# Performance work log

Measured on AMD Instinct MI355X. Metric: run time of the kernel, lower is better.

## Reference

```python
import jax, jax.numpy as jnp
import numpy as np

MAX_LORAS = 8
IN_SIZE = 4096
OUT_SIZE = 4096
B, S = 8, 1024


def setup_inputs() -> dict:
    key = jax.random.key(0)
    k1, k2, k3 = jax.random.split(key, 3)
    x = jax.random.normal(k1, (B, S, IN_SIZE), dtype=jnp.float32)
    adapter_ids = jax.random.randint(k2, (B,), 0, MAX_LORAS, dtype=jnp.int64)
    # memory_transpose=True layout: [max_loras, input_size, output_size]
    weight = jax.random.normal(k3, (MAX_LORAS, IN_SIZE, OUT_SIZE), dtype=jnp.float32) * 0.02
    return {"x": x, "adapter_ids": adapter_ids, "weight": weight}


def reference(x, adapter_ids, weight):
    # per-batch-row adapter weight gather: [B, in, out]
    w = weight[adapter_ids]
    # einsum 'bij,bjk->bik' (memory_transpose=True path)
    out = jnp.einsum('bsi,bio->bso', x, w)
    # reduce_from_tensor_model_parallel_region is identity on a single device
    return out
```

## Files before the change

kernel.cpp:

```cpp
#include <hip/hip_runtime.h>
#include <hip/hip_bf16.h>

typedef __attribute__((ext_vector_type(8))) short short8;
typedef __attribute__((ext_vector_type(4))) float f32x4;

constexpr int S_DIM   = 1024;
constexpr int IN_DIM  = 4096;
constexpr int OUT_DIM = 4096;
constexpr int NLORA   = 8;

typedef __attribute__((address_space(3))) unsigned char lds_byte_t;
typedef const __attribute__((address_space(1))) unsigned char glb_byte_t;

__device__ __forceinline__ unsigned short f2bf(float a) {
    union { __hip_bfloat16 h; unsigned short u; } c;
    c.h = __float2bfloat16(a);
    return c.u;
}
__device__ __forceinline__ unsigned int bf2pk(float a, float b) {
    return (unsigned int)f2bf(a) | ((unsigned int)f2bf(b) << 16);
}

constexpr int WBLKS = NLORA * 64 * 64;
constexpr int XBLKS = 2048;

__global__ __launch_bounds__(256)
void prep_all(const float* __restrict__ w, unsigned short* __restrict__ wt,
              const float* __restrict__ x, unsigned short* __restrict__ xb,
              const int* __restrict__ aids, int nb, int n8) {
    const int bid = blockIdx.x;
    const int tid = threadIdx.x;

    if (bid >= WBLKS) {
        const int xb0 = bid - WBLKS;
        const int stride = XBLKS * 256;
        for (int i = xb0 * 256 + tid; i < n8; i += stride) {
            const size_t o = (size_t)i * 8;
            f32x4 v0 = *reinterpret_cast<const f32x4*>(x + o);
            f32x4 v1 = *reinterpret_cast<const f32x4*>(x + o + 4);
            uint4 d;
            d.x = bf2pk(v0[0], v0[1]);
            d.y = bf2pk(v0[2], v0[3]);
            d.z = bf2pk(v1[0], v1[1]);
            d.w = bf2pk(v1[2], v1[3]);
            *reinterpret_cast<uint4*>(xb + o) = d;
        }
        return;
    }

    const int a = bid >> 12;
    bool used = false;
    for (int i = 0; i < nb; ++i) used |= (aids[i] == a);
    if (!used) return;

    const int r  = bid & 4095;
    const int n0 = (r & 63) * 64;
    const int k0 = (r >> 6) * 64;

    __shared__ __align__(16) unsigned short t[64][72];
    const float* wb = w + (size_t)a * IN_DIM * OUT_DIM;

    const int nl = (tid & 15) * 4;
    #pragma unroll
    for (int p = 0; p < 4; ++p) {
        const int kl = p * 16 + (tid >> 4);
        f32x4 v = *reinterpret_cast<const f32x4*>(wb + (size_t)(k0 + kl) * OUT_DIM + n0 + nl);
        t[nl + 0][kl] = f2bf(v[0]);
        t[nl + 1][kl] = f2bf(v[1]);
        t[nl + 2][kl] = f2bf(v[2]);
        t[nl + 3][kl] = f2bf(v[3]);
    }
    __syncthreads();
    unsigned short* wtb = wt + (size_t)a * IN_DIM * OUT_DIM;
    const int chunk = tid & 7;
    #pragma unroll
    for (int q = 0; q < 2; ++q) {
        const int row = q * 32 + (tid >> 3);
        uint4 d = *reinterpret_cast<const uint4*>(&t[row][chunk * 8]);
        *reinterpret_cast<uint4*>(wtb + (size_t)(n0 + row) * IN_DIM + k0 + chunk * 8) = d;
    }
}

constexpr int BM = 256;
constexpr int BN = 256;
constexpr int BK = 64;
constexpr int NT = IN_DIM / BK;

__global__ __launch_bounds__(512, 2)
void gemm8p(const unsigned short* __restrict__ xb, const unsigned short* __restrict__ wt,
            const int* __restrict__ aids, float* __restrict__ out) {
    __shared__ __align__(16) unsigned char lds[2][65536];

    const int bid = blockIdx.x;
    const int swz = (bid & 7) * 64 + (bid >> 3);
    const int bz  = swz >> 6;
    const int rem = swz & 63;
    const int by  = rem >> 4;
    const int bx  = rem & 15;

    const int tid  = threadIdx.x;
    const int lane = tid & 63;
    const int wid  = tid >> 6;
    const int bm0  = by * BM;
    const int bn0  = bx * BN;
    const int aid  = aids[bz];

    const unsigned short* Ab = xb + ((size_t)bz * S_DIM + bm0) * IN_DIM;
    const unsigned short* Bb = wt + (size_t)aid * IN_DIM * OUT_DIM + (size_t)bn0 * IN_DIM;

    const int wr  = (wid >> 2) * 128;
    const int wc  = (wid & 3) * 64;
    const int l15 = lane & 15;
    const int lk  = lane >> 4;

    const int rl   = lane >> 3;
    const int ksrc = ((lane & 7) ^ rl) << 3;

    f32x4 acc[8][4] = {};

    auto stageA = [&](int buf, int k0, int g) {
        #pragma unroll
        for (int c = 0; c < 2; ++c) {
            const int chunk = c * 16 + g * 8 + wid;
            const int row   = chunk * 8 + rl;
            __builtin_amdgcn_global_load_lds(
                (glb_byte_t*)(Ab + (size_t)row * IN_DIM + k0 + ksrc),
                (lds_byte_t*)(&lds[buf][chunk * 1024]), 16, 0, 0);
        }
    };
    auto stageB = [&](int buf, int k0, int g) {
        #pragma unroll
        for (int c = 0; c < 2; ++c) {
            const int chunk = (wid >> 1) * 8 + g * 4 + (wid & 1) * 2 + c;
            const int row   = chunk * 8 + rl;
            __builtin_amdgcn_global_load_lds(
                (glb_byte_t*)(Bb + (size_t)row * IN_DIM + k0 + ksrc),
                (lds_byte_t*)(&lds[buf][32768 + chunk * 1024]), 16, 0, 0);
        }
    };

    auto readA = [&](int buf, int mh, short8 (&af)[4][2]) {
        #pragma unroll
        for (int i = 0; i < 4; ++i) {
            const int row = wr + mh * 64 + i * 16 + l15;
            #pragma unroll
            for (int kc = 0; kc < 2; ++kc) {
                const int kb = kc * 64 + lk * 16;
                af[i][kc] = *reinterpret_cast<const short8*>(
                    &lds[buf][row * 128 + (kb ^ ((row & 7) << 4))]);
            }
        }
    };
    auto readB = [&](int buf, int np, short8 (&bf)[2][2]) {
        #pragma unroll
        for (int nn = 0; nn < 2; ++nn) {
            const int row = wc + np * 32 + nn * 16 + l15;
            #pragma unroll
            for (int kc = 0; kc < 2; ++kc) {
                const int kb = kc * 64 + lk * 16;
                bf[nn][kc] = *reinterpret_cast<const short8*>(
                    &lds[buf][32768 + row * 128 + (kb ^ ((row & 7) << 4))]);
            }
        }
    };

    auto qmfma = [&](short8 (&af)[4][2], short8 (&bf)[2][2], int mh, int np) {
        __builtin_amdgcn_s_setprio(1);
        #pragma unroll
        for (int i = 0; i < 4; ++i)
            #pragma unroll
            for (int nn = 0; nn < 2; ++nn)
                #pragma unroll
                for (int kc = 0; kc < 2; ++kc)
                    acc[mh * 4 + i][np * 2 + nn] = __builtin_amdgcn_mfma_f32_16x16x32_bf16(
                        af[i][kc], bf[nn][kc], acc[mh * 4 + i][np * 2 + nn], 0, 0, 0);
        __builtin_amdgcn_s_setprio(0);
    };

    stageA(0, 0, 0); stageA(0, 0, 1); stageB(0, 0, 0); stageB(0, 0, 1);
    stageA(1, BK, 0); stageA(1, BK, 1); stageB(1, BK, 0); stageB(1, BK, 1);
    asm volatile("s_waitcnt vmcnt(8)" ::: "memory");
    __builtin_amdgcn_sched_barrier(0);
    __builtin_amdgcn_s_barrier();

    short8 a0[4][2], a1[4][2], b0[2][2], b1[2][2];

    #pragma unroll 1
    for (int j = 0; j < NT; ++j) {
        const int rb = j & 1;
        const int k2 = (j + 2) * BK;
        const bool pre = (j < NT - 2);

        readA(rb, 0, a0);
        readB(rb, 0, b0);
        __builtin_amdgcn_s_barrier();
        qmfma(a0, b0, 0, 0);
        __builtin_amdgcn_s_barrier();

        readB(rb, 1, b1);
        if (pre) stageB(rb, k2, 0);
        __builtin_amdgcn_sched_barrier(0);
        __builtin_amdgcn_s_barrier();
        qmfma(a0, b1, 0, 1);
        __builtin_amdgcn_s_barrier();

        readA(rb, 1, a1);
        if (pre) stageA(rb, k2, 0);
        __builtin_amdgcn_sched_barrier(0);
        __builtin_amdgcn_s_barrier();
        qmfma(a1, b1, 1, 1);
        __builtin_amdgcn_s_barrier();

        if (pre) {
            stageB(rb, k2, 1);
            stageA(rb, k2, 1);
            asm volatile("s_waitcnt vmcnt(8)" ::: "memory");
        } else if (j == NT - 2) {
            asm volatile("s_waitcnt vmcnt(0)" ::: "memory");
        }
        __builtin_amdgcn_sched_barrier(0);
        __builtin_amdgcn_s_barrier();
        qmfma(a1, b0, 1, 0);
        __builtin_amdgcn_s_barrier();
    }

    float* obase = out + ((size_t)bz * S_DIM + bm0 + wr) * OUT_DIM + bn0 + wc;
    #pragma unroll
    for (int m = 0; m < 8; ++m) {
        #pragma unroll
        for (int n = 0; n < 4; ++n) {
            const int col = n * 16 + l15;
            #pragma unroll
            for (int r = 0; r < 4; ++r) {
                obase[(size_t)(m * 16 + lk * 4 + r) * OUT_DIM + col] = acc[m][n][r];
            }
        }
    }
}

constexpr int TMf = 128, TNf = 128, TKf = 64;
__global__ __launch_bounds__(256, 2)
void mlora_gemm(const float* __restrict__ x, const int* __restrict__ aids,
                const float* __restrict__ w, float* __restrict__ out) {
    __shared__ __align__(16) unsigned char Asf[TMf * TKf * 2];
    __shared__ __align__(16) unsigned char Bsf[TNf * TKf * 2];

    const int tid  = threadIdx.x;
    const int lane = tid & 63;
    const int wid  = tid >> 6;
    const int bn0  = blockIdx.x * TNf;
    const int bm0  = blockIdx.y * TMf;
    const int bb   = blockIdx.z;
    const int aid  = aids[bb];

    const float* Abase = x + ((size_t)bb * S_DIM + bm0) * IN_DIM;
    const float* Bbase = w + (size_t)aid * IN_DIM * OUT_DIM + bn0;

    const int wr = (wid >> 1) * 64;
    const int wc = (wid & 1) * 64;

    f32x4 acc[4][4] = {};

    const int a_row4 = tid >> 4;
    const int a_k    = (tid & 15) * 4;
    const int b_n  = tid & 127;
    const int b_k0 = (tid >> 7) * 8;
    const int l15 = lane & 15;
    const int lk  = lane >> 4;

    for (int k0 = 0; k0 < IN_DIM; k0 += TKf) {
        #pragma unroll
        for (int p = 0; p < 8; ++p) {
            const int row = p * 16 + a_row4;
            f32x4 v = *reinterpret_cast<const f32x4*>(Abase + (size_t)row * IN_DIM + (k0 + a_k));
            uint2 d;
            d.x = bf2pk(v[0], v[1]);
            d.y = bf2pk(v[2], v[3]);
            const int off = row * (TKf * 2) + ((a_k * 2) ^ ((row & 7) << 4));
            *reinterpret_cast<uint2*>(&Asf[off]) = d;
        }
        {
            const float* bp = Bbase + (size_t)(k0 + b_k0) * OUT_DIM + b_n;
            #pragma unroll
            for (int g = 0; g < 4; ++g) {
                float f0 = bp[(size_t)(g * 16 + 0) * OUT_DIM];
                float f1 = bp[(size_t)(g * 16 + 1) * OUT_DIM];
                float f2 = bp[(size_t)(g * 16 + 2) * OUT_DIM];
                float f3 = bp[(size_t)(g * 16 + 3) * OUT_DIM];
                float f4 = bp[(size_t)(g * 16 + 4) * OUT_DIM];
                float f5 = bp[(size_t)(g * 16 + 5) * OUT_DIM];
                float f6 = bp[(size_t)(g * 16 + 6) * OUT_DIM];
                float f7 = bp[(size_t)(g * 16 + 7) * OUT_DIM];
                uint4 d;
                d.x = bf2pk(f0, f1);
                d.y = bf2pk(f2, f3);
                d.z = bf2pk(f4, f5);
                d.w = bf2pk(f6, f7);
                const int ks = b_k0 + g * 16;
                const int off = b_n * (TKf * 2) + ((ks * 2) ^ ((b_n & 7) << 4));
                *reinterpret_cast<uint4*>(&Bsf[off]) = d;
            }
        }
        __syncthreads();
        #pragma unroll
        for (int kc = 0; kc < 2; ++kc) {
            const int kbyte = kc * 64 + lk * 16;
            short8 af[4], bfr[4];
            #pragma unroll
            for (int m = 0; m < 4; ++m) {
                const int row = wr + m * 16 + l15;
                af[m] = *reinterpret_cast<const short8*>(&Asf[row * (TKf * 2) + (kbyte ^ ((row & 7) << 4))]);
            }
            #pragma unroll
            for (int n = 0; n < 4; ++n) {
                const int row = wc + n * 16 + l15;
                bfr[n] = *reinterpret_cast<const short8*>(&Bsf[row * (TKf * 2) + (kbyte ^ ((row & 7) << 4))]);
            }
            #pragma unroll
            for (int m = 0; m < 4; ++m) {
                #pragma unroll
                for (int n = 0; n < 4; ++n) {
                    acc[m][n] = __builtin_amdgcn_mfma_f32_16x16x32_bf16(af[m], bfr[n], acc[m][n], 0, 0, 0);
                }
            }
        }
        __syncthreads();
    }

    float* obase = out + ((size_t)bb * S_DIM + bm0 + wr) * OUT_DIM + bn0 + wc;
    #pragma unroll
    for (int m = 0; m < 4; ++m) {
        #pragma unroll
        for (int n = 0; n < 4; ++n) {
            const int col = n * 16 + l15;
            #pragma unroll
            for (int r = 0; r < 4; ++r) {
                obase[(size_t)(m * 16 + lk * 4 + r) * OUT_DIM + col] = acc[m][n][r];
            }
        }
    }
}

extern "C" void kernel_launch(void* const* d_in, const int* in_sizes, int n_in,
                              void* d_out, int out_size, void* d_ws, size_t ws_size,
                              hipStream_t stream) {
    const float* x    = (const float*)d_in[0];
    const int*   aids = (const int*)d_in[1];
    const float* w    = (const float*)d_in[2];
    float* out = (float*)d_out;
    const int nb = in_sizes[1];

    const size_t WT_BYTES = (size_t)NLORA * IN_DIM * OUT_DIM * 2;
    const size_t XB_BYTES = (size_t)nb * S_DIM * IN_DIM * 2;

    if (ws_size >= WT_BYTES + XB_BYTES) {
        unsigned short* wt = (unsigned short*)d_ws;
        unsigned short* xbuf = (unsigned short*)((char*)d_ws + WT_BYTES);

        const int n8 = nb * S_DIM * IN_DIM / 8;
        prep_all<<<WBLKS + XBLKS, 256, 0, stream>>>(w, wt, x, xbuf, aids, nb, n8);

        const int nwg = nb * (S_DIM / BM) * (OUT_DIM / BN);
        gemm8p<<<nwg, 512, 0, stream>>>(xbuf, wt, aids, out);
    } else {
        dim3 grid(OUT_DIM / TNf, S_DIM / TMf, nb);
        mlora_gemm<<<grid, 256, 0, stream>>>(x, aids, w, out);
    }
}
```

Before: 356.3 us.

## Fuse x fp32-to-bf16 conversion into GEMM A-tile staging

```diff
diff --git a/kernel.cpp b/kernel.cpp
--- a/kernel.cpp
+++ b/kernel.cpp
@@ -22,31 +22,12 @@
 }
 
 constexpr int WBLKS = NLORA * 64 * 64;
-constexpr int XBLKS = 2048;
 
 __global__ __launch_bounds__(256)
-void prep_all(const float* __restrict__ w, unsigned short* __restrict__ wt,
-              const float* __restrict__ x, unsigned short* __restrict__ xb,
-              const int* __restrict__ aids, int nb, int n8) {
+void prep_w(const float* __restrict__ w, unsigned short* __restrict__ wt,
+            const int* __restrict__ aids, int nb) {
     const int bid = blockIdx.x;
     const int tid = threadIdx.x;
-
-    if (bid >= WBLKS) {
-        const int xb0 = bid - WBLKS;
-        const int stride = XBLKS * 256;
-        for (int i = xb0 * 256 + tid; i < n8; i += stride) {
-            const size_t o = (size_t)i * 8;
-            f32x4 v0 = *reinterpret_cast<const f32x4*>(x + o);
-            f32x4 v1 = *reinterpret_cast<const f32x4*>(x + o + 4);
-            uint4 d;
-            d.x = bf2pk(v0[0], v0[1]);
-            d.y = bf2pk(v0[2], v0[3]);
-            d.z = bf2pk(v1[0], v1[1]);
-            d.w = bf2pk(v1[2], v1[3]);
-            *reinterpret_cast<uint4*>(xb + o) = d;
-        }
-        return;
-    }
 
     const int a = bid >> 12;
     bool used = false;
@@ -87,7 +68,7 @@
 constexpr int NT = IN_DIM / BK;
 
 __global__ __launch_bounds__(512, 2)
-void gemm8p(const unsigned short* __restrict__ xb, const unsigned short* __restrict__ wt,
+void gemm8p(const float* __restrict__ x, const unsigned short* __restrict__ wt,
             const int* __restrict__ aids, float* __restrict__ out) {
     __shared__ __align__(16) unsigned char lds[2][65536];
 
@@ -105,37 +86,51 @@
     const int bn0  = bx * BN;
     const int aid  = aids[bz];
 
-    const unsigned short* Ab = xb + ((size_t)bz * S_DIM + bm0) * IN_DIM;
+    const float* Ax = x + ((size_t)bz * S_DIM + bm0) * IN_DIM;
     const unsigned short* Bb = wt + (size_t)aid * IN_DIM * OUT_DIM + (size_t)bn0 * IN_DIM;
 
     const int wr  = (wid >> 2) * 128;
     const int wc  = (wid & 3) * 64;
     const int l15 = lane & 15;
     const int lk  = lane >> 4;
-
-    const int rl   = lane >> 3;
-    const int ksrc = ((lane & 7) ^ rl) << 3;
+    const int rl  = lane >> 3;
+    const int l7  = lane & 7;
+    const int ksrcB = (l7 ^ rl) << 3;
 
     f32x4 acc[8][4] = {};
 
-    auto stageA = [&](int buf, int k0, int g) {
-        #pragma unroll
-        for (int c = 0; c < 2; ++c) {
-            const int chunk = c * 16 + g * 8 + wid;
-            const int row   = chunk * 8 + rl;
-            __builtin_amdgcn_global_load_lds(
-                (glb_byte_t*)(Ab + (size_t)row * IN_DIM + k0 + ksrc),
-                (lds_byte_t*)(&lds[buf][chunk * 1024]), 16, 0, 0);
-        }
-    };
     auto stageB = [&](int buf, int k0, int g) {
         #pragma unroll
         for (int c = 0; c < 2; ++c) {
             const int chunk = (wid >> 1) * 8 + g * 4 + (wid & 1) * 2 + c;
             const int row   = chunk * 8 + rl;
             __builtin_amdgcn_global_load_lds(
-                (glb_byte_t*)(Bb + (size_t)row * IN_DIM + k0 + ksrc),
+                (glb_byte_t*)(Bb + (size_t)row * IN_DIM + k0 + ksrcB),
                 (lds_byte_t*)(&lds[buf][32768 + chunk * 1024]), 16, 0, 0);
+        }
+    };
+
+    auto issueXA = [&](int k0, int g, f32x4 (&v)[4]) {
+        #pragma unroll
+        for (int c = 0; c < 2; ++c) {
+            const int chunk = c * 16 + g * 8 + wid;
+            const int row   = chunk * 8 + rl;
+            const float* p = Ax + (size_t)row * IN_DIM + k0 + l7 * 8;
+            v[c * 2 + 0] = *reinterpret_cast<const f32x4*>(p);
+            v[c * 2 + 1] = *reinterpret_cast<const f32x4*>(p + 4);
+        }
+    };
+    auto writeXA = [&](int buf, int g, f32x4 (&v)[4]) {
+        #pragma unroll
+        for (int c = 0; c < 2; ++c) {
+            const int chunk = c * 16 + g * 8 + wid;
+            uint4 d;
+            d.x = bf2pk(v[c * 2][0], v[c * 2][1]);
+            d.y = bf2pk(v[c * 2][2], v[c * 2][3]);
+            d.z = bf2pk(v[c * 2 + 1][0], v[c * 2 + 1][1]);
+            d.w = bf2pk(v[c * 2 + 1][2], v[c * 2 + 1][3]);
+            const int off = chunk * 1024 + rl * 128 + (((l7 ^ rl)) << 4);
+            *reinterpret_cast<uint4*>(&lds[buf][off]) = d;
         }
     };
 
@@ -177,9 +172,19 @@
         __builtin_amdgcn_s_setprio(0);
     };
 
-    stageA(0, 0, 0); stageA(0, 0, 1); stageB(0, 0, 0); stageB(0, 0, 1);
-    stageA(1, BK, 0); stageA(1, BK, 1); stageB(1, BK, 0); stageB(1, BK, 1);
-    asm volatile("s_waitcnt vmcnt(8)" ::: "memory");
+    f32x4 xa0[4], xa1[4];
+
+    issueXA(0, 0, xa0); issueXA(0, 1, xa1);
+    __builtin_amdgcn_sched_barrier(0);
+    stageB(0, 0, 0); stageB(0, 0, 1);
+    __builtin_amdgcn_sched_barrier(0);
+    writeXA(0, 0, xa0); writeXA(0, 1, xa1);
+    issueXA(BK, 0, xa0); issueXA(BK, 1, xa1);
+    __builtin_amdgcn_sched_barrier(0);
+    stageB(1, BK, 0); stageB(1, BK, 1);
+    __builtin_amdgcn_sched_barrier(0);
+    writeXA(1, 0, xa0); writeXA(1, 1, xa1);
+    asm volatile("s_waitcnt lgkmcnt(0)" ::: "memory");
     __builtin_amdgcn_sched_barrier(0);
     __builtin_amdgcn_s_barrier();
 
@@ -193,31 +198,34 @@
 
         readA(rb, 0, a0);
         readB(rb, 0, b0);
+        if (pre) issueXA(k2, 0, xa0);
+        __builtin_amdgcn_sched_barrier(0);
         __builtin_amdgcn_s_barrier();
         qmfma(a0, b0, 0, 0);
         __builtin_amdgcn_s_barrier();
 
         readB(rb, 1, b1);
+        if (pre) { writeXA(rb, 0, xa0); issueXA(k2, 1, xa1); }
+        asm volatile("s_waitcnt lgkmcnt(0)" ::: "memory");
+        __builtin_amdgcn_sched_barrier(0);
+        __builtin_amdgcn_s_barrier();
+        qmfma(a0, b1, 0, 1);
+        __builtin_amdgcn_s_barrier();
+
+        readA(rb, 1, a1);
         if (pre) stageB(rb, k2, 0);
         __builtin_amdgcn_sched_barrier(0);
         __builtin_amdgcn_s_barrier();
-        qmfma(a0, b1, 0, 1);
-        __builtin_amdgcn_s_barrier();
-
-        readA(rb, 1, a1);
-        if (pre) stageA(rb, k2, 0);
-        __builtin_amdgcn_sched_barrier(0);
-        __builtin_amdgcn_s_barrier();
         qmfma(a1, b1, 1, 1);
         __builtin_amdgcn_s_barrier();
 
         if (pre) {
+            writeXA(rb, 1, xa1);
             stageB(rb, k2, 1);
-            stageA(rb, k2, 1);
-            asm volatile("s_waitcnt vmcnt(8)" ::: "memory");
         } else if (j == NT - 2) {
             asm volatile("s_waitcnt vmcnt(0)" ::: "memory");
         }
+        asm volatile("s_waitcnt lgkmcnt(0)" ::: "memory");
         __builtin_amdgcn_sched_barrier(0);
         __builtin_amdgcn_s_barrier();
         qmfma(a1, b0, 1, 0);
@@ -351,17 +359,14 @@
     const int nb = in_sizes[1];
 
     const size_t WT_BYTES = (size_t)NLORA * IN_DIM * OUT_DIM * 2;
-    const size_t XB_BYTES = (size_t)nb * S_DIM * IN_DIM * 2;
-
-    if (ws_size >= WT_BYTES + XB_BYTES) {
+
+    if (ws_size >= WT_BYTES) {
         unsigned short* wt = (unsigned short*)d_ws;
-        unsigned short* xbuf = (unsigned short*)((char*)d_ws + WT_BYTES);
-
-        const int n8 = nb * S_DIM * IN_DIM / 8;
-        prep_all<<<WBLKS + XBLKS, 256, 0, stream>>>(w, wt, x, xbuf, aids, nb, n8);
+
+        prep_w<<<WBLKS, 256, 0, stream>>>(w, wt, aids, nb);
 
         const int nwg = nb * (S_DIM / BM) * (OUT_DIM / BN);
-        gemm8p<<<nwg, 512, 0, stream>>>(xbuf, wt, aids, out);
+        gemm8p<<<nwg, 512, 0, stream>>>(x, wt, aids, out);
     } else {
         dim3 grid(OUT_DIM / TNf, S_DIM / TMf, nb);
         mlora_gemm<<<grid, 256, 0, stream>>>(x, aids, w, out);
```

Result: slower. 520.6 us (+46.1%).
